# Optimization experiments

Hardware: AMD Instinct MI355X
Metric: run time of the kernel (lower is better)

Reference implementation:

```python
import jax, jax.numpy as jnp
import numpy as np
from jax.ops import segment_sum

N_NODES = 100000
N_EDGES = 1600000
N_GRAPHS = 2048
VOCAB = 1000
EMBED = 64
HID = 64
N_CL = 2


def setup_inputs() -> dict:
    key = jax.random.key(0)
    ks = jax.random.split(key, 9)
    x = jax.random.randint(ks[0], (N_NODES,), 0, VOCAB)
    edge_index = jax.random.randint(ks[1], (2, N_EDGES), 0, N_NODES)
    batch = jnp.sort(jax.random.randint(ks[2], (N_NODES,), 0, N_GRAPHS))
    emb = jax.random.normal(ks[3], (VOCAB, EMBED), dtype=jnp.float32)
    emb = emb.at[0].set(0.0)  # padding_idx=0
    s1 = 1.0 / np.sqrt(EMBED)
    s2 = 1.0 / np.sqrt(HID)
    W1 = jax.random.uniform(ks[4], (EMBED, HID), jnp.float32, -s1, s1)
    b1 = jnp.zeros((HID,), jnp.float32)
    W2 = jax.random.uniform(ks[5], (HID, HID), jnp.float32, -s2, s2)
    b2 = jnp.zeros((HID,), jnp.float32)
    Wl = jax.random.uniform(ks[6], (HID, N_CL), jnp.float32, -s2, s2)
    bl = jax.random.uniform(ks[7], (N_CL,), jnp.float32, -s2, s2)
    return {"x": x, "edge_index": edge_index, "batch": batch,
            "emb": emb, "W1": W1, "b1": b1, "W2": W2, "b2": b2,
            "Wl": Wl, "bl": bl}


def _gcn_conv(h, row, col, norm, W, b):
    # h: [N, Fin] -> [N, Fout]; PyG GCNConv: lin -> gather -> norm -> scatter-add -> bias
    h = h @ W
    msg = h[row] * norm[:, None]          # [E+N, Fout] gathered, normalized messages
    out = segment_sum(msg, col, num_segments=N_NODES)
    return out + b


def reference(x, edge_index, batch, emb, W1, b1, W2, b2, Wl, bl):
    # add self loops (GCNConv default)
    loop = jnp.arange(N_NODES)
    row = jnp.concatenate([edge_index[0], loop])  # sources
    col = jnp.concatenate([edge_index[1], loop])  # targets
    # symmetric normalization: deg^{-1/2}[row] * deg^{-1/2}[col]
    deg = segment_sum(jnp.ones_like(col, dtype=jnp.float32), col, num_segments=N_NODES)
    dinv = jnp.where(deg > 0, jax.lax.rsqrt(jnp.maximum(deg, 1.0)), 0.0)
    norm = dinv[row] * dinv[col]

    h = emb[x]                                        # [N, EMBED]
    h = jax.nn.relu(_gcn_conv(h, row, col, norm, W1, b1))
    h = jax.nn.relu(_gcn_conv(h, row, col, norm, W2, b2))

    # global mean pool over graphs
    sums = segment_sum(h, batch, num_segments=N_GRAPHS)          # [G, HID]
    cnts = segment_sum(jnp.ones((N_NODES,), jnp.float32), batch, num_segments=N_GRAPHS)
    pooled = sums / jnp.maximum(cnts, 1.0)[:, None]
    return pooled @ Wl + bl                                      # [G, N_CL]
```

## Files before the change

### kernel.cpp

```cpp
#include <hip/hip_runtime.h>
#include <hip/hip_fp16.h>

#define N_NODES  100000
#define N_EDGES  1600000
#define N_GRAPHS 2048
#define VOCAB    1000
#define EMBED    64
#define HID      64
#define N_CL     2
#define CAP      64
#define NBLK     391
#define EBLK4    1563
#define NQUAD    400000
#define VBLK     63
#define NSWEEP   8
#define RANGE    12500

typedef __half2 h2;
typedef int i4 __attribute__((ext_vector_type(4)));

__device__ inline uint2 pack_h4(float4 a) {
    h2 lo = __float22half2_rn(make_float2(a.x, a.y));
    h2 hi = __float22half2_rn(make_float2(a.z, a.w));
    uint2 r;
    r.x = *reinterpret_cast<unsigned*>(&lo);
    r.y = *reinterpret_cast<unsigned*>(&hi);
    return r;
}

__device__ inline void acc_h8(h2 acc[4], uint4 raw) {
    acc[0] = __hadd2(acc[0], *reinterpret_cast<h2*>(&raw.x));
    acc[1] = __hadd2(acc[1], *reinterpret_cast<h2*>(&raw.y));
    acc[2] = __hadd2(acc[2], *reinterpret_cast<h2*>(&raw.z));
    acc[3] = __hadd2(acc[3], *reinterpret_cast<h2*>(&raw.w));
}

__device__ inline void h8_to_f(const h2 acc[4], float4& A, float4& B) {
    float2 f0 = __half22float2(acc[0]);
    float2 f1 = __half22float2(acc[1]);
    float2 f2 = __half22float2(acc[2]);
    float2 f3 = __half22float2(acc[3]);
    A.x = f0.x; A.y = f0.y; A.z = f1.x; A.w = f1.y;
    B.x = f2.x; B.y = f2.y; B.z = f3.x; B.w = f3.y;
}

__device__ inline void xor_reduce8(float4& A, float4& B) {
#pragma unroll
    for (int m = 8; m <= 32; m <<= 1) {
        A.x += __shfl_xor(A.x, m, 64); A.y += __shfl_xor(A.y, m, 64);
        A.z += __shfl_xor(A.z, m, 64); A.w += __shfl_xor(A.w, m, 64);
        B.x += __shfl_xor(B.x, m, 64); B.y += __shfl_xor(B.y, m, 64);
        B.z += __shfl_xor(B.z, m, 64); B.w += __shfl_xor(B.w, m, 64);
    }
}

__device__ inline void gather2(const uint4* __restrict__ tn,
                               const int* __restrict__ sl0, const int* __restrict__ sl1,
                               int n0, int n1, int es, int fg, h2 a0[4], h2 a1[4]) {
    int base = es * 4;
    int4 q0 = ((const int4*)sl0)[es];
    int4 q1 = ((const int4*)sl1)[es];
    if (base + 0 < n0) acc_h8(a0, tn[q0.x * 8 + fg]);
    if (base + 0 < n1) acc_h8(a1, tn[q1.x * 8 + fg]);
    if (base + 1 < n0) acc_h8(a0, tn[q0.y * 8 + fg]);
    if (base + 1 < n1) acc_h8(a1, tn[q1.y * 8 + fg]);
    if (base + 2 < n0) acc_h8(a0, tn[q0.z * 8 + fg]);
    if (base + 2 < n1) acc_h8(a1, tn[q1.z * 8 + fg]);
    if (base + 3 < n0) acc_h8(a0, tn[q0.w * 8 + fg]);
    if (base + 3 < n1) acc_h8(a1, tn[q1.w * 8 + fg]);
    if (n0 > 32 || n1 > 32) {
        int b2 = 32 + es * 4;
        int4 p0 = ((const int4*)sl0)[8 + es];
        int4 p1 = ((const int4*)sl1)[8 + es];
        if (b2 + 0 < n0) acc_h8(a0, tn[p0.x * 8 + fg]);
        if (b2 + 0 < n1) acc_h8(a1, tn[p1.x * 8 + fg]);
        if (b2 + 1 < n0) acc_h8(a0, tn[p0.y * 8 + fg]);
        if (b2 + 1 < n1) acc_h8(a1, tn[p1.y * 8 + fg]);
        if (b2 + 2 < n0) acc_h8(a0, tn[p0.z * 8 + fg]);
        if (b2 + 2 < n1) acc_h8(a1, tn[p1.z * 8 + fg]);
        if (b2 + 3 < n0) acc_h8(a0, tn[p0.w * 8 + fg]);
        if (b2 + 3 < n1) acc_h8(a1, tn[p1.w * 8 + fg]);
    }
}

__global__ __launch_bounds__(256) void k_fill_slots(const int* __restrict__ row, const int* __restrict__ col,
                                                    int* __restrict__ cnt, int* __restrict__ slots,
                                                    const int* __restrict__ batch, int* __restrict__ start,
                                                    const float* __restrict__ emb, const float* __restrict__ W1,
                                                    float* __restrict__ E) {
    int bid = blockIdx.x;
    if (bid < NSWEEP * EBLK4) {
        int sweep = bid & (NSWEEP - 1);
        int t = (bid >> 3) * 256 + threadIdx.x;
        if (t >= NQUAD) return;
        i4 c4 = __builtin_nontemporal_load((const i4*)col + t);
        i4 r4 = __builtin_nontemporal_load((const i4*)row + t);
        unsigned lo = (unsigned)(sweep * RANGE);
        if ((unsigned)(c4.x - lo) < (unsigned)RANGE) { int pos = atomicAdd(&cnt[c4.x], 1); if (pos < CAP) slots[c4.x * CAP + pos] = r4.x; }
        if ((unsigned)(c4.y - lo) < (unsigned)RANGE) { int pos = atomicAdd(&cnt[c4.y], 1); if (pos < CAP) slots[c4.y * CAP + pos] = r4.y; }
        if ((unsigned)(c4.z - lo) < (unsigned)RANGE) { int pos = atomicAdd(&cnt[c4.z], 1); if (pos < CAP) slots[c4.z * CAP + pos] = r4.z; }
        if ((unsigned)(c4.w - lo) < (unsigned)RANGE) { int pos = atomicAdd(&cnt[c4.w], 1); if (pos < CAP) slots[c4.w * CAP + pos] = r4.w; }
    } else if (bid < NSWEEP * EBLK4 + NBLK) {
        int v = (bid - NSWEEP * EBLK4) * 256 + threadIdx.x;
        if (v >= N_NODES) return;
        int b = batch[v];
        int pb = (v == 0) ? -1 : batch[v - 1];
        for (int g = pb + 1; g <= b; ++g) start[g] = v;
        if (v == N_NODES - 1)
            for (int g = b + 1; g <= N_GRAPHS; ++g) start[g] = N_NODES;
    } else {
        int t = (bid - NSWEEP * EBLK4 - NBLK) * 256 + threadIdx.x;
        int j = t >> 4;
        int f4 = t & 15;
        if (j >= VOCAB) return;
        const float4* W4 = (const float4*)W1;
        const float* er = emb + j * EMBED;
        float4 acc = make_float4(0.f, 0.f, 0.f, 0.f);
#pragma unroll 8
        for (int k = 0; k < EMBED; ++k) {
            float hv = er[k];
            float4 w = W4[k * 16 + f4];
            acc.x += hv * w.x; acc.y += hv * w.y; acc.z += hv * w.z; acc.w += hv * w.w;
        }
        ((float4*)E)[t] = acc;
    }
}

__global__ __launch_bounds__(256) void k_tn1(const int* __restrict__ x, const int* __restrict__ cnt,
                                             const float* __restrict__ E, uint2* __restrict__ tn) {
    int t = blockIdx.x * 256 + threadIdx.x;
    int v = t >> 4;
    int f4 = t & 15;
    float d = rsqrtf((float)(cnt[v] + 1));
    float4 a = ((const float4*)E)[x[v] * 16 + f4];
    a.x *= d; a.y *= d; a.z *= d; a.w *= d;
    tn[t] = pack_h4(a);
}

__global__ __launch_bounds__(256) void k_agg_gemm(const uint4* __restrict__ tn,
                                                  const int* __restrict__ cnt,
                                                  const int* __restrict__ slots,
                                                  const float* __restrict__ bias,
                                                  const float* __restrict__ W2,
                                                  __half* __restrict__ tn2) {
    __shared__ float hrow[8][HID];
    int wid = threadIdx.x >> 6;
    int lane = threadIdx.x & 63;
    int fg = lane & 7;
    int es = lane >> 3;
    int v0 = blockIdx.x * 8 + wid * 2;
    int v1 = v0 + 1;
    int c0 = cnt[v0], c1 = cnt[v1];
    int n0 = min(c0, CAP), n1 = min(c1, CAP);
    h2 z = __float2half2_rn(0.f);
    h2 a0[4] = {z, z, z, z};
    h2 a1[4] = {z, z, z, z};
    if (es == 0) acc_h8(a0, tn[v0 * 8 + fg]);
    if (es == 1) acc_h8(a1, tn[v1 * 8 + fg]);
    gather2(tn, slots + v0 * CAP, slots + v1 * CAP, n0, n1, es, fg, a0, a1);
    float4 a0A, a0B, a1A, a1B;
    h8_to_f(a0, a0A, a0B);
    h8_to_f(a1, a1A, a1B);
    xor_reduce8(a0A, a0B);
    xor_reduce8(a1A, a1B);
    float d0 = rsqrtf((float)(c0 + 1));
    float d1 = rsqrtf((float)(c1 + 1));
    float4 bA = ((const float4*)bias)[fg * 2 + 0];
    float4 bB = ((const float4*)bias)[fg * 2 + 1];
    if (es == 0) {
        float4 oA, oB;
        oA.x = fmaxf(d0 * a0A.x + bA.x, 0.f); oA.y = fmaxf(d0 * a0A.y + bA.y, 0.f);
        oA.z = fmaxf(d0 * a0A.z + bA.z, 0.f); oA.w = fmaxf(d0 * a0A.w + bA.w, 0.f);
        oB.x = fmaxf(d0 * a0B.x + bB.x, 0.f); oB.y = fmaxf(d0 * a0B.y + bB.y, 0.f);
        oB.z = fmaxf(d0 * a0B.z + bB.z, 0.f); oB.w = fmaxf(d0 * a0B.w + bB.w, 0.f);
        ((float4*)&hrow[wid * 2][fg * 8])[0] = oA;
        ((float4*)&hrow[wid * 2][fg * 8])[1] = oB;
    }
    if (es == 1) {
        float4 oA, oB;
        oA.x = fmaxf(d1 * a1A.x + bA.x, 0.f); oA.y = fmaxf(d1 * a1A.y + bA.y, 0.f);
        oA.z = fmaxf(d1 * a1A.z + bA.z, 0.f); oA.w = fmaxf(d1 * a1A.w + bA.w, 0.f);
        oB.x = fmaxf(d1 * a1B.x + bB.x, 0.f); oB.y = fmaxf(d1 * a1B.y + bB.y, 0.f);
        oB.z = fmaxf(d1 * a1B.z + bB.z, 0.f); oB.w = fmaxf(d1 * a1B.w + bB.w, 0.f);
        ((float4*)&hrow[wid * 2 + 1][fg * 8])[0] = oA;
        ((float4*)&hrow[wid * 2 + 1][fg * 8])[1] = oB;
    }
    __syncthreads();
    const float4* h04 = (const float4*)hrow[wid * 2];
    const float4* h14 = (const float4*)hrow[wid * 2 + 1];
    float s0 = 0.f, s1 = 0.f;
#pragma unroll 4
    for (int k4 = 0; k4 < 16; ++k4) {
        float4 ha = h04[k4];
        float4 hb = h14[k4];
        int k = k4 * 4;
        float w0 = W2[(k + 0) * HID + lane];
        float w1 = W2[(k + 1) * HID + lane];
        float w2 = W2[(k + 2) * HID + lane];
        float w3 = W2[(k + 3) * HID + lane];
        s0 += ha.x * w0 + ha.y * w1 + ha.z * w2 + ha.w * w3;
        s1 += hb.x * w0 + hb.y * w1 + hb.z * w2 + hb.w * w3;
    }
    tn2[v0 * HID + lane] = __float2half(d0 * s0);
    tn2[v1 * HID + lane] = __float2half(d1 * s1);
}

__global__ __launch_bounds__(256) void k_agg(const uint4* __restrict__ tn,
                                             const int* __restrict__ cnt,
                                             const int* __restrict__ slots,
                                             const float* __restrict__ bias,
                                             float* __restrict__ h) {
    int wid = threadIdx.x >> 6;
    int lane = threadIdx.x & 63;
    int fg = lane & 7;
    int es = lane >> 3;
    int v0 = blockIdx.x * 8 + wid * 2;
    int v1 = v0 + 1;
    int c0 = cnt[v0], c1 = cnt[v1];
    int n0 = min(c0, CAP), n1 = min(c1, CAP);
    h2 z = __float2half2_rn(0.f);
    h2 a0[4] = {z, z, z, z};
    h2 a1[4] = {z, z, z, z};
    if (es == 0) acc_h8(a0, tn[v0 * 8 + fg]);
    if (es == 1) acc_h8(a1, tn[v1 * 8 + fg]);
    gather2(tn, slots + v0 * CAP, slots + v1 * CAP, n0, n1, es, fg, a0, a1);
    float4 a0A, a0B, a1A, a1B;
    h8_to_f(a0, a0A, a0B);
    h8_to_f(a1, a1A, a1B);
    xor_reduce8(a0A, a0B);
    xor_reduce8(a1A, a1B);
    float4 bA = ((const float4*)bias)[fg * 2 + 0];
    float4 bB = ((const float4*)bias)[fg * 2 + 1];
    if (es == 0) {
        float d0 = rsqrtf((float)(c0 + 1));
        float4 oA, oB;
        oA.x = fmaxf(d0 * a0A.x + bA.x, 0.f); oA.y = fmaxf(d0 * a0A.y + bA.y, 0.f);
        oA.z = fmaxf(d0 * a0A.z + bA.z, 0.f); oA.w = fmaxf(d0 * a0A.w + bA.w, 0.f);
        oB.x = fmaxf(d0 * a0B.x + bB.x, 0.f); oB.y = fmaxf(d0 * a0B.y + bB.y, 0.f);
        oB.z = fmaxf(d0 * a0B.z + bB.z, 0.f); oB.w = fmaxf(d0 * a0B.w + bB.w, 0.f);
        ((float4*)&h[v0 * HID + fg * 8])[0] = oA;
        ((float4*)&h[v0 * HID + fg * 8])[1] = oB;
    }
    if (es == 1) {
        float d1 = rsqrtf((float)(c1 + 1));
        float4 oA, oB;
        oA.x = fmaxf(d1 * a1A.x + bA.x, 0.f); oA.y = fmaxf(d1 * a1A.y + bA.y, 0.f);
        oA.z = fmaxf(d1 * a1A.z + bA.z, 0.f); oA.w = fmaxf(d1 * a1A.w + bA.w, 0.f);
        oB.x = fmaxf(d1 * a1B.x + bB.x, 0.f); oB.y = fmaxf(d1 * a1B.y + bB.y, 0.f);
        oB.z = fmaxf(d1 * a1B.z + bB.z, 0.f); oB.w = fmaxf(d1 * a1B.w + bB.w, 0.f);
        ((float4*)&h[v1 * HID + fg * 8])[0] = oA;
        ((float4*)&h[v1 * HID + fg * 8])[1] = oB;
    }
}

__global__ __launch_bounds__(256) void k_pool_out(const float* __restrict__ h,
                                                  const int* __restrict__ start,
                                                  const float* __restrict__ Wl,
                                                  const float* __restrict__ bl,
                                                  float* __restrict__ out) {
    int g = (blockIdx.x * 256 + threadIdx.x) >> 6;
    int f = threadIdx.x & 63;
    if (g >= N_GRAPHS) return;
    int s = start[g], e = start[g + 1];
    float acc = 0.f;
    int v = s;
    for (; v + 4 <= e; v += 4) {
        float a0 = h[(v + 0) * HID + f];
        float a1 = h[(v + 1) * HID + f];
        float a2 = h[(v + 2) * HID + f];
        float a3 = h[(v + 3) * HID + f];
        acc += (a0 + a1) + (a2 + a3);
    }
    for (; v < e; ++v) acc += h[v * HID + f];
    float m = acc / fmaxf((float)(e - s), 1.f);
    float p0 = m * Wl[f * N_CL + 0];
    float p1 = m * Wl[f * N_CL + 1];
#pragma unroll
    for (int off = 32; off > 0; off >>= 1) {
        p0 += __shfl_down(p0, off, 64);
        p1 += __shfl_down(p1, off, 64);
    }
    if (f == 0) {
        out[g * N_CL + 0] = p0 + bl[0];
        out[g * N_CL + 1] = p1 + bl[1];
    }
}

extern "C" void kernel_launch(void* const* d_in, const int* in_sizes, int n_in,
                              void* d_out, int out_size, void* d_ws, size_t ws_size,
                              hipStream_t stream) {
    const int*   x     = (const int*)d_in[0];
    const int*   ei    = (const int*)d_in[1];
    const int*   batch = (const int*)d_in[2];
    const float* emb   = (const float*)d_in[3];
    const float* W1    = (const float*)d_in[4];
    const float* b1    = (const float*)d_in[5];
    const float* W2    = (const float*)d_in[6];
    const float* b2    = (const float*)d_in[7];
    const float* Wl    = (const float*)d_in[8];
    const float* bl    = (const float*)d_in[9];
    float* out = (float*)d_out;

    const int* row = ei;
    const int* col = ei + N_EDGES;

    char* ws = (char*)d_ws;
    size_t off = 0;
    auto alloc = [&](size_t bytes) { char* p = ws + off; off = (off + bytes + 511) & ~(size_t)511; return p; };
    const size_t FEAT_BYTES  = (size_t)N_NODES * HID * sizeof(float);
    const size_t FEATH_BYTES = (size_t)N_NODES * HID * sizeof(__half);
    float* A      = (float*)alloc(FEAT_BYTES);
    __half* Bt    = (__half*)alloc(FEATH_BYTES);
    int*   slots  = (int*)  alloc((size_t)N_NODES * CAP * sizeof(int));
    float* E      = (float*)alloc((size_t)VOCAB * HID * sizeof(float));
    int*   start  = (int*)  alloc((size_t)(N_GRAPHS + 1) * sizeof(int));
    int*   cnt    = (int*)  alloc((size_t)N_NODES * sizeof(int));

    dim3 blk(256);
    dim3 g_fill(NSWEEP * EBLK4 + NBLK + VBLK);
    dim3 g_tn1(N_NODES * 16 / 256);
    dim3 g_agg(N_NODES / 8);
    dim3 g_po((N_GRAPHS * 64 + 255) / 256);

    hipMemsetAsync(cnt, 0, (size_t)N_NODES * sizeof(int), stream);

    k_fill_slots<<<g_fill, blk, 0, stream>>>(row, col, cnt, slots, batch, start, emb, W1, E);

    k_tn1<<<g_tn1, blk, 0, stream>>>(x, cnt, E, (uint2*)A);

    k_agg_gemm<<<g_agg, blk, 0, stream>>>((const uint4*)A, cnt, slots, b1, W2, Bt);

    k_agg<<<g_agg, blk, 0, stream>>>((const uint4*)Bt, cnt, slots, b2, A);

    k_pool_out<<<g_po, blk, 0, stream>>>(A, start, Wl, bl, out);
}
```

Measured before the change: 277.4 us.

## Fuse all pipeline stages into one persistent cooperative kernel with grid syncs

Replaces the memset and five separate kernel launches with one cooperative persistent kernel. It loops each stage over virtual blocks and separates the stages with grid-wide barriers. The intent is to remove launch gaps and per-kernel tail effects. In exchange, grid size is capped by occupancy, which limits latency hiding for the atomic-heavy fill and gather phases, and grid.sync adds its own cost. The old multi-kernel path stays as a fallback if the cooperative launch fails.

```diff
diff --git a/kernel.cpp b/kernel.cpp
--- a/kernel.cpp
+++ b/kernel.cpp
@@ -1,5 +1,8 @@
 #include <hip/hip_runtime.h>
 #include <hip/hip_fp16.h>
+#include <hip/hip_cooperative_groups.h>
+
+namespace cg = cooperative_groups;
 
 #define N_NODES  100000
 #define N_EDGES  1600000
@@ -15,6 +18,10 @@
 #define VBLK     63
 #define NSWEEP   8
 #define RANGE    12500
+#define FILLBLK  (NSWEEP * EBLK4 + NBLK + VBLK)
+#define TN1BLK   (N_NODES * 16 / 256)
+#define AGGBLK   (N_NODES / 8)
+#define POBLK    (N_GRAPHS * 64 / 256)
 
 typedef __half2 h2;
 typedef int i4 __attribute__((ext_vector_type(4)));
@@ -80,6 +87,227 @@
         if (b2 + 2 < n1) acc_h8(a1, tn[p1.z * 8 + fg]);
         if (b2 + 3 < n0) acc_h8(a0, tn[p0.w * 8 + fg]);
         if (b2 + 3 < n1) acc_h8(a1, tn[p1.w * 8 + fg]);
+    }
+}
+
+
+__global__ __launch_bounds__(256, 8) void k_fused(
+    const int* __restrict__ row, const int* __restrict__ col,
+    const int* __restrict__ x, const int* __restrict__ batch,
+    const float* __restrict__ emb, const float* __restrict__ W1,
+    const float* __restrict__ b1, const float* __restrict__ W2,
+    const float* __restrict__ b2, const float* __restrict__ Wl,
+    const float* __restrict__ bl, float* __restrict__ E,
+    int* __restrict__ cnt, int* __restrict__ slots, int* __restrict__ start,
+    float* __restrict__ A, __half* __restrict__ Bt, float* __restrict__ out)
+{
+    cg::grid_group grid = cg::this_grid();
+    const int nb = gridDim.x;
+    const int tid = threadIdx.x;
+    __shared__ float hrow[8][HID];
+
+    for (int i = blockIdx.x * 256 + tid; i < N_NODES; i += nb * 256) cnt[i] = 0;
+    grid.sync();
+
+    for (int vb = blockIdx.x; vb < FILLBLK; vb += nb) {
+        if (vb < NSWEEP * EBLK4) {
+            int sweep = vb & (NSWEEP - 1);
+            int t = (vb >> 3) * 256 + tid;
+            if (t < NQUAD) {
+                i4 c4 = __builtin_nontemporal_load((const i4*)col + t);
+                i4 r4 = __builtin_nontemporal_load((const i4*)row + t);
+                unsigned lo = (unsigned)(sweep * RANGE);
+                if ((unsigned)(c4.x - lo) < (unsigned)RANGE) { int pos = atomicAdd(&cnt[c4.x], 1); if (pos < CAP) slots[c4.x * CAP + pos] = r4.x; }
+                if ((unsigned)(c4.y - lo) < (unsigned)RANGE) { int pos = atomicAdd(&cnt[c4.y], 1); if (pos < CAP) slots[c4.y * CAP + pos] = r4.y; }
+                if ((unsigned)(c4.z - lo) < (unsigned)RANGE) { int pos = atomicAdd(&cnt[c4.z], 1); if (pos < CAP) slots[c4.z * CAP + pos] = r4.z; }
+                if ((unsigned)(c4.w - lo) < (unsigned)RANGE) { int pos = atomicAdd(&cnt[c4.w], 1); if (pos < CAP) slots[c4.w * CAP + pos] = r4.w; }
+            }
+        } else if (vb < NSWEEP * EBLK4 + NBLK) {
+            int v = (vb - NSWEEP * EBLK4) * 256 + tid;
+            if (v < N_NODES) {
+                int b = batch[v];
+                int pb = (v == 0) ? -1 : batch[v - 1];
+                for (int g = pb + 1; g <= b; ++g) start[g] = v;
+                if (v == N_NODES - 1)
+                    for (int g = b + 1; g <= N_GRAPHS; ++g) start[g] = N_NODES;
+            }
+        } else {
+            int t = (vb - NSWEEP * EBLK4 - NBLK) * 256 + tid;
+            int j = t >> 4;
+            int f4 = t & 15;
+            if (j < VOCAB) {
+                const float4* W4 = (const float4*)W1;
+                const float* er = emb + j * EMBED;
+                float4 acc = make_float4(0.f, 0.f, 0.f, 0.f);
+#pragma unroll 8
+                for (int k = 0; k < EMBED; ++k) {
+                    float hv = er[k];
+                    float4 w = W4[k * 16 + f4];
+                    acc.x += hv * w.x; acc.y += hv * w.y; acc.z += hv * w.z; acc.w += hv * w.w;
+                }
+                ((float4*)E)[t] = acc;
+            }
+        }
+    }
+    grid.sync();
+
+    {
+        uint2* tn1w = (uint2*)A;
+        for (int vb = blockIdx.x; vb < TN1BLK; vb += nb) {
+            int t = vb * 256 + tid;
+            int v = t >> 4;
+            int f4 = t & 15;
+            float d = rsqrtf((float)(cnt[v] + 1));
+            float4 a = ((const float4*)E)[x[v] * 16 + f4];
+            a.x *= d; a.y *= d; a.z *= d; a.w *= d;
+            tn1w[t] = pack_h4(a);
+        }
+    }
+    grid.sync();
+
+    {
+        const uint4* tn = (const uint4*)A;
+        int wid = tid >> 6;
+        int lane = tid & 63;
+        int fg = lane & 7;
+        int es = lane >> 3;
+        for (int vb = blockIdx.x; vb < AGGBLK; vb += nb) {
+            int v0 = vb * 8 + wid * 2;
+            int v1 = v0 + 1;
+            int c0 = cnt[v0], c1 = cnt[v1];
+            int n0 = min(c0, CAP), n1 = min(c1, CAP);
+            h2 z = __float2half2_rn(0.f);
+            h2 a0[4] = {z, z, z, z};
+            h2 a1[4] = {z, z, z, z};
+            if (es == 0) acc_h8(a0, tn[v0 * 8 + fg]);
+            if (es == 1) acc_h8(a1, tn[v1 * 8 + fg]);
+            gather2(tn, slots + v0 * CAP, slots + v1 * CAP, n0, n1, es, fg, a0, a1);
+            float4 a0A, a0B, a1A, a1B;
+            h8_to_f(a0, a0A, a0B);
+            h8_to_f(a1, a1A, a1B);
+            xor_reduce8(a0A, a0B);
+            xor_reduce8(a1A, a1B);
+            float d0 = rsqrtf((float)(c0 + 1));
+            float d1 = rsqrtf((float)(c1 + 1));
+            float4 bA = ((const float4*)b1)[fg * 2 + 0];
+            float4 bB = ((const float4*)b1)[fg * 2 + 1];
+            if (es == 0) {
+                float4 oA, oB;
+                oA.x = fmaxf(d0 * a0A.x + bA.x, 0.f); oA.y = fmaxf(d0 * a0A.y + bA.y, 0.f);
+                oA.z = fmaxf(d0 * a0A.z + bA.z, 0.f); oA.w = fmaxf(d0 * a0A.w + bA.w, 0.f);
+                oB.x = fmaxf(d0 * a0B.x + bB.x, 0.f); oB.y = fmaxf(d0 * a0B.y + bB.y, 0.f);
+                oB.z = fmaxf(d0 * a0B.z + bB.z, 0.f); oB.w = fmaxf(d0 * a0B.w + bB.w, 0.f);
+                ((float4*)&hrow[wid * 2][fg * 8])[0] = oA;
+                ((float4*)&hrow[wid * 2][fg * 8])[1] = oB;
+            }
+            if (es == 1) {
+                float4 oA, oB;
+                oA.x = fmaxf(d1 * a1A.x + bA.x, 0.f); oA.y = fmaxf(d1 * a1A.y + bA.y, 0.f);
+                oA.z = fmaxf(d1 * a1A.z + bA.z, 0.f); oA.w = fmaxf(d1 * a1A.w + bA.w, 0.f);
+                oB.x = fmaxf(d1 * a1B.x + bB.x, 0.f); oB.y = fmaxf(d1 * a1B.y + bB.y, 0.f);
+                oB.z = fmaxf(d1 * a1B.z + bB.z, 0.f); oB.w = fmaxf(d1 * a1B.w + bB.w, 0.f);
+                ((float4*)&hrow[wid * 2 + 1][fg * 8])[0] = oA;
+                ((float4*)&hrow[wid * 2 + 1][fg * 8])[1] = oB;
+            }
+            __syncthreads();
+            const float4* h04 = (const float4*)hrow[wid * 2];
+            const float4* h14 = (const float4*)hrow[wid * 2 + 1];
+            float s0 = 0.f, s1 = 0.f;
+#pragma unroll 4
+            for (int k4 = 0; k4 < 16; ++k4) {
+                float4 ha = h04[k4];
+                float4 hb = h14[k4];
+                int k = k4 * 4;
+                float w0 = W2[(k + 0) * HID + lane];
+                float w1 = W2[(k + 1) * HID + lane];
+                float w2 = W2[(k + 2) * HID + lane];
+                float w3 = W2[(k + 3) * HID + lane];
+                s0 += ha.x * w0 + ha.y * w1 + ha.z * w2 + ha.w * w3;
+                s1 += hb.x * w0 + hb.y * w1 + hb.z * w2 + hb.w * w3;
+            }
+            Bt[v0 * HID + lane] = __float2half(d0 * s0);
+            Bt[v1 * HID + lane] = __float2half(d1 * s1);
+            __syncthreads();
+        }
+    }
+    grid.sync();
+
+    {
+        const uint4* tn = (const uint4*)Bt;
+        int wid = tid >> 6;
+        int lane = tid & 63;
+        int fg = lane & 7;
+        int es = lane >> 3;
+        for (int vb = blockIdx.x; vb < AGGBLK; vb += nb) {
+            int v0 = vb * 8 + wid * 2;
+            int v1 = v0 + 1;
+            int c0 = cnt[v0], c1 = cnt[v1];
+            int n0 = min(c0, CAP), n1 = min(c1, CAP);
+            h2 z = __float2half2_rn(0.f);
+            h2 a0[4] = {z, z, z, z};
+            h2 a1[4] = {z, z, z, z};
+            if (es == 0) acc_h8(a0, tn[v0 * 8 + fg]);
+            if (es == 1) acc_h8(a1, tn[v1 * 8 + fg]);
+            gather2(tn, slots + v0 * CAP, slots + v1 * CAP, n0, n1, es, fg, a0, a1);
+            float4 a0A, a0B, a1A, a1B;
+            h8_to_f(a0, a0A, a0B);
+            h8_to_f(a1, a1A, a1B);
+            xor_reduce8(a0A, a0B);
+            xor_reduce8(a1A, a1B);
+            float4 bA = ((const float4*)b2)[fg * 2 + 0];
+            float4 bB = ((const float4*)b2)[fg * 2 + 1];
+            if (es == 0) {
+                float d0 = rsqrtf((float)(c0 + 1));
+                float4 oA, oB;
+                oA.x = fmaxf(d0 * a0A.x + bA.x, 0.f); oA.y = fmaxf(d0 * a0A.y + bA.y, 0.f);
+                oA.z = fmaxf(d0 * a0A.z + bA.z, 0.f); oA.w = fmaxf(d0 * a0A.w + bA.w, 0.f);
+                oB.x = fmaxf(d0 * a0B.x + bB.x, 0.f); oB.y = fmaxf(d0 * a0B.y + bB.y, 0.f);
+                oB.z = fmaxf(d0 * a0B.z + bB.z, 0.f); oB.w = fmaxf(d0 * a0B.w + bB.w, 0.f);
+                ((float4*)&A[v0 * HID + fg * 8])[0] = oA;
+                ((float4*)&A[v0 * HID + fg * 8])[1] = oB;
+            }
+            if (es == 1) {
+                float d1 = rsqrtf((float)(c1 + 1));
+                float4 oA, oB;
+                oA.x = fmaxf(d1 * a1A.x + bA.x, 0.f); oA.y = fmaxf(d1 * a1A.y + bA.y, 0.f);
+                oA.z = fmaxf(d1 * a1A.z + bA.z, 0.f); oA.w = fmaxf(d1 * a1A.w + bA.w, 0.f);
+                oB.x = fmaxf(d1 * a1B.x + bB.x, 0.f); oB.y = fmaxf(d1 * a1B.y + bB.y, 0.f);
+                oB.z = fmaxf(d1 * a1B.z + bB.z, 0.f); oB.w = fmaxf(d1 * a1B.w + bB.w, 0.f);
+                ((float4*)&A[v1 * HID + fg * 8])[0] = oA;
+                ((float4*)&A[v1 * HID + fg * 8])[1] = oB;
+            }
+        }
+    }
+    grid.sync();
+
+    for (int vb = blockIdx.x; vb < POBLK; vb += nb) {
+        int g = vb * 4 + (tid >> 6);
+        int f = tid & 63;
+        if (g < N_GRAPHS) {
+            int s = start[g], e = start[g + 1];
+            float acc = 0.f;
+            int v = s;
+            for (; v + 4 <= e; v += 4) {
+                float q0 = A[(v + 0) * HID + f];
+                float q1 = A[(v + 1) * HID + f];
+                float q2 = A[(v + 2) * HID + f];
+                float q3 = A[(v + 3) * HID + f];
+                acc += (q0 + q1) + (q2 + q3);
+            }
+            for (; v < e; ++v) acc += A[v * HID + f];
+            float m = acc / fmaxf((float)(e - s), 1.f);
+            float p0 = m * Wl[f * N_CL + 0];
+            float p1 = m * Wl[f * N_CL + 1];
+#pragma unroll
+            for (int off = 32; off > 0; off >>= 1) {
+                p0 += __shfl_down(p0, off, 64);
+                p1 += __shfl_down(p1, off, 64);
+            }
+            if (f == 0) {
+                out[g * N_CL + 0] = p0 + bl[0];
+                out[g * N_CL + 1] = p1 + bl[1];
+            }
+        }
     }
 }
 
@@ -316,21 +544,29 @@
     int*   start  = (int*)  alloc((size_t)(N_GRAPHS + 1) * sizeof(int));
     int*   cnt    = (int*)  alloc((size_t)N_NODES * sizeof(int));
 
-    dim3 blk(256);
-    dim3 g_fill(NSWEEP * EBLK4 + NBLK + VBLK);
-    dim3 g_tn1(N_NODES * 16 / 256);
-    dim3 g_agg(N_NODES / 8);
-    dim3 g_po((N_GRAPHS * 64 + 255) / 256);
-
-    hipMemsetAsync(cnt, 0, (size_t)N_NODES * sizeof(int), stream);
-
-    k_fill_slots<<<g_fill, blk, 0, stream>>>(row, col, cnt, slots, batch, start, emb, W1, E);
-
-    k_tn1<<<g_tn1, blk, 0, stream>>>(x, cnt, E, (uint2*)A);
-
-    k_agg_gemm<<<g_agg, blk, 0, stream>>>((const uint4*)A, cnt, slots, b1, W2, Bt);
-
-    k_agg<<<g_agg, blk, 0, stream>>>((const uint4*)Bt, cnt, slots, b2, A);
-
-    k_pool_out<<<g_po, blk, 0, stream>>>(A, start, Wl, bl, out);
-}
+    int maxPerCU = 0;
+    hipError_t qe = hipOccupancyMaxActiveBlocksPerMultiprocessor(&maxPerCU, k_fused, 256, 0);
+    int nb = 2048;
+    if (qe == hipSuccess && maxPerCU > 0) {
+        int cap = maxPerCU * 256;
+        if (cap < nb) nb = cap;
+    }
+    void* args[] = {(void*)&row, (void*)&col, (void*)&x, (void*)&batch, (void*)&emb, (void*)&W1,
+                    (void*)&b1, (void*)&W2, (void*)&b2, (void*)&Wl, (void*)&bl, (void*)&E,
+                    (void*)&cnt, (void*)&slots, (void*)&start, (void*)&A, (void*)&Bt, (void*)&out};
+    hipError_t le = hipLaunchCooperativeKernel((const void*)k_fused, dim3(nb), dim3(256), args, 0, stream);
+
+    if (le != hipSuccess) {
+        dim3 blk(256);
+        dim3 g_fill(FILLBLK);
+        dim3 g_tn1(TN1BLK);
+        dim3 g_agg(AGGBLK);
+        dim3 g_po(POBLK);
+        hipMemsetAsync(cnt, 0, (size_t)N_NODES * sizeof(int), stream);
+        k_fill_slots<<<g_fill, blk, 0, stream>>>(row, col, cnt, slots, batch, start, emb, W1, E);
+        k_tn1<<<g_tn1, blk, 0, stream>>>(x, cnt, E, (uint2*)A);
+        k_agg_gemm<<<g_agg, blk, 0, stream>>>((const uint4*)A, cnt, slots, b1, W2, Bt);
+        k_agg<<<g_agg, blk, 0, stream>>>((const uint4*)Bt, cnt, slots, b2, A);
+        k_pool_out<<<g_po, blk, 0, stream>>>(A, start, Wl, bl, out);
+    }
+}
```

After: 880.7 us. +217.5%, slower.
